# Kernel tuning notes

Measured on AMD Instinct MI355X. Metric: run time of the kernel, lower is better.

## Reference

```python
import jax, jax.numpy as jnp
import numpy as np

N_NODES = 200_000
N_EDGES = 6_400_000
N_GRAPHS = 512


def _sage_conv(x, edge_index, Wl, bl, Wr):
    """PyG SAGEConv (mean aggr): lin_l(mean_j x_j) + lin_r(x_i).
    lin_l has bias, lin_r does not. Messages flow src -> dst."""
    src, dst = edge_index[0], edge_index[1]
    n = x.shape[0]
    # gather neighbor features [E, F] and segment-mean into dst nodes
    msg_sum = jax.ops.segment_sum(x[src], dst, num_segments=n)
    deg = jax.ops.segment_sum(jnp.ones((src.shape[0],), x.dtype), dst, num_segments=n)
    mean = msg_sum / jnp.maximum(deg, 1.0)[:, None]  # zero in-degree -> 0
    return mean @ Wl.T + bl + x @ Wr.T


def setup_inputs() -> dict:
    key = jax.random.key(0)
    ks = jax.random.split(key, 9)
    x = jax.random.normal(ks[0], (N_NODES, 1), dtype=jnp.float32)
    edge_index = jax.random.randint(ks[1], (2, N_EDGES), 0, N_NODES, dtype=jnp.int64)
    batch = jnp.sort(jax.random.randint(ks[2], (N_NODES,), 0, N_GRAPHS, dtype=jnp.int64))
    W1l = jax.random.normal(ks[3], (16, 1), dtype=jnp.float32)
    b1 = jax.random.normal(ks[4], (16,), dtype=jnp.float32)
    W1r = jax.random.normal(ks[5], (16, 1), dtype=jnp.float32)
    W2l = jax.random.normal(ks[6], (1, 16), dtype=jnp.float32)
    b2 = jax.random.normal(ks[7], (1,), dtype=jnp.float32)
    W2r = jax.random.normal(ks[8], (1, 16), dtype=jnp.float32)
    return {"x": x, "edge_index": edge_index, "batch": batch, "batch_size": N_GRAPHS,
            "W1l": W1l, "b1": b1, "W1r": W1r, "W2l": W2l, "b2": b2, "W2r": W2r}


def reference(x, edge_index, batch, batch_size, W1l, b1, W1r, W2l, b2, W2r):
    h = _sage_conv(x, edge_index, W1l, b1, W1r)          # [N, 16]
    h = jax.nn.relu(h)
    h = _sage_conv(h, edge_index, W2l, b2, W2r)          # [N, 1]
    # global_add_pool: segment-sum node features by graph id
    out = jax.ops.segment_sum(h, batch, num_segments=batch_size)  # [B, 1]
    return out
```

## Files before the change

### kernel.cpp

```cpp
#include <hip/hip_runtime.h>


#define PARTS     512
#define BLK       1024
#define EPT       8
#define TILE      (BLK * EPT)
#define PGRID     512
#define BINSMAX   400
#define LDSHIFT   9
#define LDMASK    511u
#define CNT_ONE   (1u << 25)
#define FX_BIAS   131072
#define SCALE     4096.0f
#define INV_SCALE (1.0f / 4096.0f)

__global__ __launch_bounds__(BLK) void partition_kernel(
    const int* __restrict__ ei, unsigned* __restrict__ pairs,
    unsigned* __restrict__ tails, int E, int bins, unsigned Mdiv, int cap,
    int T) {
    __shared__ unsigned hist[PARTS], curs[PARTS], gbase[PARTS];
    const int tid = threadIdx.x;

    for (int t = blockIdx.x; t < T; t += PGRID) {
        for (int j = tid; j < PARTS; j += BLK) { hist[j] = 0; curs[j] = 0; }
        __syncthreads();

        int eb = t * TILE + tid * EPT;
        int nv = E - eb; nv = nv < 0 ? 0 : (nv > EPT ? EPT : nv);
        int srcv[EPT], dstv[EPT];
        if (nv == EPT && ((E & 3) == 0)) {
            const int4* s4 = (const int4*)(ei + eb);
            const int4* d4 = (const int4*)(ei + E + eb);
            int4 a = s4[0], b = s4[1];
            srcv[0] = a.x; srcv[1] = a.y; srcv[2] = a.z; srcv[3] = a.w;
            srcv[4] = b.x; srcv[5] = b.y; srcv[6] = b.z; srcv[7] = b.w;
            int4 c = d4[0], d = d4[1];
            dstv[0] = c.x; dstv[1] = c.y; dstv[2] = c.z; dstv[3] = c.w;
            dstv[4] = d.x; dstv[5] = d.y; dstv[6] = d.z; dstv[7] = d.w;
        } else {
            for (int k = 0; k < nv; ++k) {
                srcv[k] = ei[eb + k]; dstv[k] = ei[E + eb + k];
            }
        }

        unsigned w[EPT]; int pt[EPT];
#pragma unroll
        for (int k = 0; k < EPT; ++k) {
            if (k < nv) {
                unsigned dst = (unsigned)dstv[k];
                unsigned pp = (unsigned)(((unsigned long long)dst * Mdiv) >> 32);
                int ld = (int)dst - (int)pp * bins;
                while (ld >= bins) { ld -= bins; ++pp; }
                while (ld < 0)     { ld += bins; --pp; }
                pt[k] = (int)pp;
                w[k] = ((unsigned)srcv[k] << LDSHIFT) | (unsigned)ld;
                atomicAdd(&hist[pp], 1u);
            }
        }
        __syncthreads();

        if (tid < PARTS) {
            unsigned h = hist[tid];
            gbase[tid] = h ? atomicAdd(&tails[tid], h) : 0u;
        }
        __syncthreads();

#pragma unroll
        for (int k = 0; k < EPT; ++k) {
            if (k < nv) {
                unsigned slot = atomicAdd(&curs[pt[k]], 1u);
                unsigned idx = gbase[pt[k]] + slot;
                if (idx < (unsigned)cap)
                    pairs[(size_t)pt[k] * cap + idx] = w[k];
            }
        }
        __syncthreads();
    }
}

__global__ __launch_bounds__(BLK) void bin1_kernel(
    const unsigned* __restrict__ pairs, const unsigned* __restrict__ tails,
    const float* __restrict__ x,
    const float* __restrict__ W1l, const float* __restrict__ b1,
    const float* __restrict__ W1r, const float* __restrict__ W2l,
    const float* __restrict__ W2r,
    float* __restrict__ deg, float* __restrict__ pv, float* __restrict__ qv,
    int N, int bins, int cap) {
    __shared__ unsigned sb[BINSMAX];
    __shared__ float s_w1l[16], s_b1[16], s_w1r[16], s_w2l[16], s_w2r[16];
    const int tid = threadIdx.x;
    const int p = blockIdx.x;
    if (tid < 16) {
        s_w1l[tid] = W1l[tid]; s_b1[tid] = b1[tid]; s_w1r[tid] = W1r[tid];
        s_w2l[tid] = W2l[tid]; s_w2r[tid] = W2r[tid];
    }
    for (int j = tid; j < bins; j += BLK) sb[j] = 0;
    __syncthreads();

    int len = (int)tails[p]; if (len > cap) len = cap;
    const unsigned* bp = pairs + (size_t)p * cap;
    int n4 = len >> 2;
    const uint4* bp4 = (const uint4*)bp;
    for (int e = tid; e < n4; e += BLK) {
        uint4 wq = bp4[e];
        atomicAdd(&sb[wq.x & LDMASK],
                  CNT_ONE + (unsigned)((int)rintf(x[wq.x >> LDSHIFT] * SCALE) + FX_BIAS));
        atomicAdd(&sb[wq.y & LDMASK],
                  CNT_ONE + (unsigned)((int)rintf(x[wq.y >> LDSHIFT] * SCALE) + FX_BIAS));
        atomicAdd(&sb[wq.z & LDMASK],
                  CNT_ONE + (unsigned)((int)rintf(x[wq.z >> LDSHIFT] * SCALE) + FX_BIAS));
        atomicAdd(&sb[wq.w & LDMASK],
                  CNT_ONE + (unsigned)((int)rintf(x[wq.w >> LDSHIFT] * SCALE) + FX_BIAS));
    }
    for (int e = (n4 << 2) + tid; e < len; e += BLK) {
        unsigned wv = bp[e];
        atomicAdd(&sb[wv & LDMASK],
                  CNT_ONE + (unsigned)((int)rintf(x[wv >> LDSHIFT] * SCALE) + FX_BIAS));
    }
    __syncthreads();

    int lo = p * bins;
    int nb = N - lo; if (nb > bins) nb = bins;
    for (int j = tid; j < nb; j += BLK) {
        unsigned w = sb[j];
        unsigned c = w >> 25;
        float dg  = (float)c;
        float sum = (float)(int)((w & (CNT_ONE - 1)) - c * (unsigned)FX_BIAS) * INV_SCALE;
        float m   = sum / fmaxf(dg, 1.0f);
        float xv  = x[lo + j];
        float pa = 0.0f, qa = 0.0f;
#pragma unroll
        for (int f = 0; f < 16; ++f) {
            float h = fmaf(m, s_w1l[f], fmaf(xv, s_w1r[f], s_b1[f]));
            h = fmaxf(h, 0.0f);
            pa = fmaf(h, s_w2l[f], pa);
            qa = fmaf(h, s_w2r[f], qa);
        }
        deg[lo + j] = dg;
        pv[lo + j]  = pa;
        qv[lo + j]  = qa;
    }
}

__global__ __launch_bounds__(BLK) void bin2_kernel(
    const unsigned* __restrict__ pairs, const unsigned* __restrict__ tails,
    const float* __restrict__ pv, const float* __restrict__ deg,
    const float* __restrict__ qv, const float* __restrict__ b2,
    const int* __restrict__ batch, float* __restrict__ out,
    int N, int bins, int cap) {
    __shared__ int sbi[BINSMAX];
    const int tid = threadIdx.x;
    const int p = blockIdx.x;
    for (int j = tid; j < bins; j += BLK) sbi[j] = 0;
    __syncthreads();

    int len = (int)tails[p]; if (len > cap) len = cap;
    const unsigned* bp = pairs + (size_t)p * cap;
    int n4 = len >> 2;
    const uint4* bp4 = (const uint4*)bp;
    for (int e = tid; e < n4; e += BLK) {
        uint4 wq = bp4[e];
        atomicAdd(&sbi[wq.x & LDMASK], (int)rintf(pv[wq.x >> LDSHIFT] * SCALE));
        atomicAdd(&sbi[wq.y & LDMASK], (int)rintf(pv[wq.y >> LDSHIFT] * SCALE));
        atomicAdd(&sbi[wq.z & LDMASK], (int)rintf(pv[wq.z >> LDSHIFT] * SCALE));
        atomicAdd(&sbi[wq.w & LDMASK], (int)rintf(pv[wq.w >> LDSHIFT] * SCALE));
    }
    for (int e = (n4 << 2) + tid; e < len; e += BLK) {
        unsigned wv = bp[e];
        atomicAdd(&sbi[wv & LDMASK], (int)rintf(pv[wv >> LDSHIFT] * SCALE));
    }
    __syncthreads();

    int lo = p * bins;
    int nb = N - lo; if (nb > bins) nb = bins;
    float b2v = b2[0];
    float val = 0.0f;
    int g;
    if (tid < nb) {
        float s2 = (float)sbi[tid] * INV_SCALE;
        val = s2 / fmaxf(deg[lo + tid], 1.0f) + b2v + qv[lo + tid];
        g = batch[lo + tid];
    } else {
        g = batch[lo + nb - 1];
    }
    int g0 = __shfl(g, 0);
    unsigned long long same = __ballot(g == g0);
    if (same == ~0ULL) {
        for (int off = 32; off > 0; off >>= 1) val += __shfl_down(val, off);
        if ((tid & 63) == 0) atomicAdd(&out[g0], val);
    } else {
        atomicAdd(&out[g], val);
    }
}

extern "C" void kernel_launch(void* const* d_in, const int* in_sizes, int n_in,
                              void* d_out, int out_size, void* d_ws, size_t ws_size,
                              hipStream_t stream) {
    const float* x     = (const float*)d_in[0];
    const int*   ei    = (const int*)d_in[1];
    const int*   batch = (const int*)d_in[2];
    const float* W1l = (const float*)d_in[4];
    const float* b1  = (const float*)d_in[5];
    const float* W1r = (const float*)d_in[6];
    const float* W2l = (const float*)d_in[7];
    const float* b2  = (const float*)d_in[8];
    const float* W2r = (const float*)d_in[9];

    const int N = in_sizes[0];
    const int E = in_sizes[1] / 2;
    float* out = (float*)d_out;

    const int bins = (N + PARTS - 1) / PARTS;
    const unsigned Mdiv =
        (unsigned)(((1ULL << 32) + (unsigned)bins - 1) / (unsigned)bins);
    const int EperP = E / PARTS;
    int cap = ((EperP + EperP / 8 + 1024) + 1023) & ~1023;
    int T = (E + TILE - 1) / TILE;

    unsigned* pairs = (unsigned*)d_ws;
    float* deg = (float*)(pairs + (size_t)PARTS * cap);
    float* pv  = deg + N;
    float* qv  = pv + N;
    unsigned* tails = (unsigned*)(qv + N);

    hipMemsetAsync(d_out, 0, (size_t)out_size * sizeof(float), stream);
    hipMemsetAsync(tails, 0, PARTS * sizeof(unsigned), stream);

    partition_kernel<<<PGRID, BLK, 0, stream>>>(ei, pairs, tails,
                                                E, bins, Mdiv, cap, T);
    bin1_kernel<<<PARTS, BLK, 0, stream>>>(pairs, tails, x, W1l, b1, W1r,
                                           W2l, W2r, deg, pv, qv, N, bins, cap);
    bin2_kernel<<<PARTS, BLK, 0, stream>>>(pairs, tails, pv, deg, qv, b2,
                                           batch, out, N, bins, cap);
}
```

Measured before the change: 243.3 us.

## Embed quantized source features during partition and halve partition count

The partition pass now gathers x for each edge's source and stores a 16-bit biased fixed-point copy next to the packed edge word. Layer-1 binning then streams these values instead of doing random gathers into x. Partitions drop from 512 to 256, which doubles the bin width, and the remaining gather loops in both binning kernels are unrolled to 8 edges per thread. The per-partition capacity now comes from the workspace size, with a fallback to the old gather path; in exchange the partition pass does extra writes and x values are clamped to a 16-bit range.

```diff
diff --git a/kernel.cpp b/kernel.cpp
--- a/kernel.cpp
+++ b/kernel.cpp
@@ -1,21 +1,23 @@
 #include <hip/hip_runtime.h>
 
 
-#define PARTS     512
+#define PARTS     256
 #define BLK       1024
 #define EPT       8
 #define TILE      (BLK * EPT)
-#define PGRID     512
-#define BINSMAX   400
-#define LDSHIFT   9
-#define LDMASK    511u
+#define PGRID     256
+#define BINSMAX   800
+#define LDSHIFT   10
+#define LDMASK    1023u
 #define CNT_ONE   (1u << 25)
+#define XV_BIAS   32768
 #define FX_BIAS   131072
 #define SCALE     4096.0f
 #define INV_SCALE (1.0f / 4096.0f)
 
-__global__ __launch_bounds__(BLK) void partition_kernel(
-    const int* __restrict__ ei, unsigned* __restrict__ pairs,
+__global__ __launch_bounds__(BLK) void partition_embed_kernel(
+    const int* __restrict__ ei, const float* __restrict__ x,
+    unsigned* __restrict__ pairs, unsigned short* __restrict__ xvs,
     unsigned* __restrict__ tails, int E, int bins, unsigned Mdiv, int cap,
     int T) {
     __shared__ unsigned hist[PARTS], curs[PARTS], gbase[PARTS];
@@ -43,6 +45,10 @@
             }
         }
 
+        float xg[EPT];
+#pragma unroll
+        for (int k = 0; k < EPT; ++k) if (k < nv) xg[k] = x[srcv[k]];
+
         unsigned w[EPT]; int pt[EPT];
 #pragma unroll
         for (int k = 0; k < EPT; ++k) {
@@ -70,6 +76,70 @@
             if (k < nv) {
                 unsigned slot = atomicAdd(&curs[pt[k]], 1u);
                 unsigned idx = gbase[pt[k]] + slot;
+                if (idx < (unsigned)cap) {
+                    int xq = (int)rintf(xg[k] * SCALE) + XV_BIAS;
+                    xq = xq < 0 ? 0 : (xq > 65535 ? 65535 : xq);
+                    size_t o = (size_t)pt[k] * cap + idx;
+                    pairs[o] = w[k];
+                    xvs[o] = (unsigned short)xq;
+                }
+            }
+        }
+        __syncthreads();
+    }
+}
+
+__global__ __launch_bounds__(BLK) void partition_plain_kernel(
+    const int* __restrict__ ei, unsigned* __restrict__ pairs,
+    unsigned* __restrict__ tails, int E, int bins, unsigned Mdiv, int cap,
+    int T) {
+    __shared__ unsigned hist[PARTS], curs[PARTS], gbase[PARTS];
+    const int tid = threadIdx.x;
+    for (int t = blockIdx.x; t < T; t += PGRID) {
+        for (int j = tid; j < PARTS; j += BLK) { hist[j] = 0; curs[j] = 0; }
+        __syncthreads();
+        int eb = t * TILE + tid * EPT;
+        int nv = E - eb; nv = nv < 0 ? 0 : (nv > EPT ? EPT : nv);
+        int srcv[EPT], dstv[EPT];
+        if (nv == EPT && ((E & 3) == 0)) {
+            const int4* s4 = (const int4*)(ei + eb);
+            const int4* d4 = (const int4*)(ei + E + eb);
+            int4 a = s4[0], b = s4[1];
+            srcv[0] = a.x; srcv[1] = a.y; srcv[2] = a.z; srcv[3] = a.w;
+            srcv[4] = b.x; srcv[5] = b.y; srcv[6] = b.z; srcv[7] = b.w;
+            int4 c = d4[0], d = d4[1];
+            dstv[0] = c.x; dstv[1] = c.y; dstv[2] = c.z; dstv[3] = c.w;
+            dstv[4] = d.x; dstv[5] = d.y; dstv[6] = d.z; dstv[7] = d.w;
+        } else {
+            for (int k = 0; k < nv; ++k) {
+                srcv[k] = ei[eb + k]; dstv[k] = ei[E + eb + k];
+            }
+        }
+        unsigned w[EPT]; int pt[EPT];
+#pragma unroll
+        for (int k = 0; k < EPT; ++k) {
+            if (k < nv) {
+                unsigned dst = (unsigned)dstv[k];
+                unsigned pp = (unsigned)(((unsigned long long)dst * Mdiv) >> 32);
+                int ld = (int)dst - (int)pp * bins;
+                while (ld >= bins) { ld -= bins; ++pp; }
+                while (ld < 0)     { ld += bins; --pp; }
+                pt[k] = (int)pp;
+                w[k] = ((unsigned)srcv[k] << LDSHIFT) | (unsigned)ld;
+                atomicAdd(&hist[pp], 1u);
+            }
+        }
+        __syncthreads();
+        if (tid < PARTS) {
+            unsigned h = hist[tid];
+            gbase[tid] = h ? atomicAdd(&tails[tid], h) : 0u;
+        }
+        __syncthreads();
+#pragma unroll
+        for (int k = 0; k < EPT; ++k) {
+            if (k < nv) {
+                unsigned slot = atomicAdd(&curs[pt[k]], 1u);
+                unsigned idx = gbase[pt[k]] + slot;
                 if (idx < (unsigned)cap)
                     pairs[(size_t)pt[k] * cap + idx] = w[k];
             }
@@ -78,7 +148,78 @@
     }
 }
 
-__global__ __launch_bounds__(BLK) void bin1_kernel(
+__device__ __forceinline__ void node_phase1(
+    const unsigned* sb, const float* x,
+    const float* s_w1l, const float* s_b1, const float* s_w1r,
+    const float* s_w2l, const float* s_w2r,
+    float* deg, float* pv, float* qv, int lo, int nb, int bias) {
+    for (int j = threadIdx.x; j < nb; j += BLK) {
+        unsigned w = sb[j];
+        unsigned c = w >> 25;
+        float dg  = (float)c;
+        float sum = (float)((int)(w & (CNT_ONE - 1)) - (int)(c * (unsigned)bias))
+                    * INV_SCALE;
+        float m   = sum / fmaxf(dg, 1.0f);
+        float xv  = x[lo + j];
+        float pa = 0.0f, qa = 0.0f;
+#pragma unroll
+        for (int f = 0; f < 16; ++f) {
+            float h = fmaf(m, s_w1l[f], fmaf(xv, s_w1r[f], s_b1[f]));
+            h = fmaxf(h, 0.0f);
+            pa = fmaf(h, s_w2l[f], pa);
+            qa = fmaf(h, s_w2r[f], qa);
+        }
+        deg[lo + j] = dg;
+        pv[lo + j]  = pa;
+        qv[lo + j]  = qa;
+    }
+}
+
+__global__ __launch_bounds__(BLK) void bin1_stream_kernel(
+    const unsigned* __restrict__ pairs, const unsigned short* __restrict__ xvs,
+    const unsigned* __restrict__ tails, const float* __restrict__ x,
+    const float* __restrict__ W1l, const float* __restrict__ b1,
+    const float* __restrict__ W1r, const float* __restrict__ W2l,
+    const float* __restrict__ W2r,
+    float* __restrict__ deg, float* __restrict__ pv, float* __restrict__ qv,
+    int N, int bins, int cap) {
+    __shared__ unsigned sb[BINSMAX];
+    __shared__ float s_w1l[16], s_b1[16], s_w1r[16], s_w2l[16], s_w2r[16];
+    const int tid = threadIdx.x;
+    const int p = blockIdx.x;
+    if (tid < 16) {
+        s_w1l[tid] = W1l[tid]; s_b1[tid] = b1[tid]; s_w1r[tid] = W1r[tid];
+        s_w2l[tid] = W2l[tid]; s_w2r[tid] = W2r[tid];
+    }
+    for (int j = tid; j < bins; j += BLK) sb[j] = 0;
+    __syncthreads();
+
+    int len = (int)tails[p]; if (len > cap) len = cap;
+    const unsigned* bp = pairs + (size_t)p * cap;
+    const unsigned short* xp = xvs + (size_t)p * cap;
+    int n4 = len >> 2;
+    const uint4* bp4 = (const uint4*)bp;
+    const ushort4* xp4 = (const ushort4*)xp;
+    for (int e = tid; e < n4; e += BLK) {
+        uint4 wq = bp4[e];
+        ushort4 xw = xp4[e];
+        atomicAdd(&sb[wq.x & LDMASK], CNT_ONE + (unsigned)xw.x);
+        atomicAdd(&sb[wq.y & LDMASK], CNT_ONE + (unsigned)xw.y);
+        atomicAdd(&sb[wq.z & LDMASK], CNT_ONE + (unsigned)xw.z);
+        atomicAdd(&sb[wq.w & LDMASK], CNT_ONE + (unsigned)xw.w);
+    }
+    for (int e = (n4 << 2) + tid; e < len; e += BLK) {
+        atomicAdd(&sb[bp[e] & LDMASK], CNT_ONE + (unsigned)xp[e]);
+    }
+    __syncthreads();
+
+    int lo = p * bins;
+    int nb = N - lo; if (nb > bins) nb = bins;
+    node_phase1(sb, x, s_w1l, s_b1, s_w1r, s_w2l, s_w2r,
+                deg, pv, qv, lo, nb, XV_BIAS);
+}
+
+__global__ __launch_bounds__(BLK) void bin1_gather_kernel(
     const unsigned* __restrict__ pairs, const unsigned* __restrict__ tails,
     const float* __restrict__ x,
     const float* __restrict__ W1l, const float* __restrict__ b1,
@@ -99,20 +240,24 @@
 
     int len = (int)tails[p]; if (len > cap) len = cap;
     const unsigned* bp = pairs + (size_t)p * cap;
-    int n4 = len >> 2;
+    int n8 = len >> 3;
     const uint4* bp4 = (const uint4*)bp;
-    for (int e = tid; e < n4; e += BLK) {
-        uint4 wq = bp4[e];
-        atomicAdd(&sb[wq.x & LDMASK],
-                  CNT_ONE + (unsigned)((int)rintf(x[wq.x >> LDSHIFT] * SCALE) + FX_BIAS));
-        atomicAdd(&sb[wq.y & LDMASK],
-                  CNT_ONE + (unsigned)((int)rintf(x[wq.y >> LDSHIFT] * SCALE) + FX_BIAS));
-        atomicAdd(&sb[wq.z & LDMASK],
-                  CNT_ONE + (unsigned)((int)rintf(x[wq.z >> LDSHIFT] * SCALE) + FX_BIAS));
-        atomicAdd(&sb[wq.w & LDMASK],
-                  CNT_ONE + (unsigned)((int)rintf(x[wq.w >> LDSHIFT] * SCALE) + FX_BIAS));
-    }
-    for (int e = (n4 << 2) + tid; e < len; e += BLK) {
+    for (int i = tid; i < n8; i += BLK) {
+        uint4 a = bp4[2 * i], b = bp4[2 * i + 1];
+        float v0 = x[a.x >> LDSHIFT], v1 = x[a.y >> LDSHIFT];
+        float v2 = x[a.z >> LDSHIFT], v3 = x[a.w >> LDSHIFT];
+        float v4 = x[b.x >> LDSHIFT], v5 = x[b.y >> LDSHIFT];
+        float v6 = x[b.z >> LDSHIFT], v7 = x[b.w >> LDSHIFT];
+        atomicAdd(&sb[a.x & LDMASK], CNT_ONE + (unsigned)((int)rintf(v0 * SCALE) + FX_BIAS));
+        atomicAdd(&sb[a.y & LDMASK], CNT_ONE + (unsigned)((int)rintf(v1 * SCALE) + FX_BIAS));
+        atomicAdd(&sb[a.z & LDMASK], CNT_ONE + (unsigned)((int)rintf(v2 * SCALE) + FX_BIAS));
+        atomicAdd(&sb[a.w & LDMASK], CNT_ONE + (unsigned)((int)rintf(v3 * SCALE) + FX_BIAS));
+        atomicAdd(&sb[b.x & LDMASK], CNT_ONE + (unsigned)((int)rintf(v4 * SCALE) + FX_BIAS));
+        atomicAdd(&sb[b.y & LDMASK], CNT_ONE + (unsigned)((int)rintf(v5 * SCALE) + FX_BIAS));
+        atomicAdd(&sb[b.z & LDMASK], CNT_ONE + (unsigned)((int)rintf(v6 * SCALE) + FX_BIAS));
+        atomicAdd(&sb[b.w & LDMASK], CNT_ONE + (unsigned)((int)rintf(v7 * SCALE) + FX_BIAS));
+    }
+    for (int e = (n8 << 3) + tid; e < len; e += BLK) {
         unsigned wv = bp[e];
         atomicAdd(&sb[wv & LDMASK],
                   CNT_ONE + (unsigned)((int)rintf(x[wv >> LDSHIFT] * SCALE) + FX_BIAS));
@@ -121,25 +266,8 @@
 
     int lo = p * bins;
     int nb = N - lo; if (nb > bins) nb = bins;
-    for (int j = tid; j < nb; j += BLK) {
-        unsigned w = sb[j];
-        unsigned c = w >> 25;
-        float dg  = (float)c;
-        float sum = (float)(int)((w & (CNT_ONE - 1)) - c * (unsigned)FX_BIAS) * INV_SCALE;
-        float m   = sum / fmaxf(dg, 1.0f);
-        float xv  = x[lo + j];
-        float pa = 0.0f, qa = 0.0f;
-#pragma unroll
-        for (int f = 0; f < 16; ++f) {
-            float h = fmaf(m, s_w1l[f], fmaf(xv, s_w1r[f], s_b1[f]));
-            h = fmaxf(h, 0.0f);
-            pa = fmaf(h, s_w2l[f], pa);
-            qa = fmaf(h, s_w2r[f], qa);
-        }
-        deg[lo + j] = dg;
-        pv[lo + j]  = pa;
-        qv[lo + j]  = qa;
-    }
+    node_phase1(sb, x, s_w1l, s_b1, s_w1r, s_w2l, s_w2r,
+                deg, pv, qv, lo, nb, FX_BIAS);
 }
 
 __global__ __launch_bounds__(BLK) void bin2_kernel(
@@ -156,16 +284,24 @@
 
     int len = (int)tails[p]; if (len > cap) len = cap;
     const unsigned* bp = pairs + (size_t)p * cap;
-    int n4 = len >> 2;
+    int n8 = len >> 3;
     const uint4* bp4 = (const uint4*)bp;
-    for (int e = tid; e < n4; e += BLK) {
-        uint4 wq = bp4[e];
-        atomicAdd(&sbi[wq.x & LDMASK], (int)rintf(pv[wq.x >> LDSHIFT] * SCALE));
-        atomicAdd(&sbi[wq.y & LDMASK], (int)rintf(pv[wq.y >> LDSHIFT] * SCALE));
-        atomicAdd(&sbi[wq.z & LDMASK], (int)rintf(pv[wq.z >> LDSHIFT] * SCALE));
-        atomicAdd(&sbi[wq.w & LDMASK], (int)rintf(pv[wq.w >> LDSHIFT] * SCALE));
-    }
-    for (int e = (n4 << 2) + tid; e < len; e += BLK) {
+    for (int i = tid; i < n8; i += BLK) {
+        uint4 a = bp4[2 * i], b = bp4[2 * i + 1];
+        float v0 = pv[a.x >> LDSHIFT], v1 = pv[a.y >> LDSHIFT];
+        float v2 = pv[a.z >> LDSHIFT], v3 = pv[a.w >> LDSHIFT];
+        float v4 = pv[b.x >> LDSHIFT], v5 = pv[b.y >> LDSHIFT];
+        float v6 = pv[b.z >> LDSHIFT], v7 = pv[b.w >> LDSHIFT];
+        atomicAdd(&sbi[a.x & LDMASK], (int)rintf(v0 * SCALE));
+        atomicAdd(&sbi[a.y & LDMASK], (int)rintf(v1 * SCALE));
+        atomicAdd(&sbi[a.z & LDMASK], (int)rintf(v2 * SCALE));
+        atomicAdd(&sbi[a.w & LDMASK], (int)rintf(v3 * SCALE));
+        atomicAdd(&sbi[b.x & LDMASK], (int)rintf(v4 * SCALE));
+        atomicAdd(&sbi[b.y & LDMASK], (int)rintf(v5 * SCALE));
+        atomicAdd(&sbi[b.z & LDMASK], (int)rintf(v6 * SCALE));
+        atomicAdd(&sbi[b.w & LDMASK], (int)rintf(v7 * SCALE));
+    }
+    for (int e = (n8 << 3) + tid; e < len; e += BLK) {
         unsigned wv = bp[e];
         atomicAdd(&sbi[wv & LDMASK], (int)rintf(pv[wv >> LDSHIFT] * SCALE));
     }
@@ -213,12 +349,25 @@
     const int bins = (N + PARTS - 1) / PARTS;
     const unsigned Mdiv =
         (unsigned)(((1ULL << 32) + (unsigned)bins - 1) / (unsigned)bins);
-    const int EperP = E / PARTS;
-    int cap = ((EperP + EperP / 8 + 1024) + 1023) & ~1023;
     int T = (E + TILE - 1) / TILE;
 
+    long long wsWords = (long long)(ws_size / 4);
+    long long avail = wsWords - (3LL * N + 1024);
+    int capE = (int)((avail / 384) * 256) & ~1023;
+    capE = (int)((avail * 2 / 3) / PARTS) & ~1023;
+    bool embed = capE >= 26624;
+    int cap;
+    if (embed) {
+        cap = capE > 30720 ? 30720 : capE;
+    } else {
+        cap = (int)(avail / PARTS) & ~1023;
+        if (cap > 30720) cap = 30720;
+    }
+
     unsigned* pairs = (unsigned*)d_ws;
-    float* deg = (float*)(pairs + (size_t)PARTS * cap);
+    unsigned short* xvs = (unsigned short*)(pairs + (size_t)PARTS * cap);
+    float* deg = embed ? (float*)(xvs + (size_t)PARTS * cap)
+                       : (float*)(pairs + (size_t)PARTS * cap);
     float* pv  = deg + N;
     float* qv  = pv + N;
     unsigned* tails = (unsigned*)(qv + N);
@@ -226,10 +375,19 @@
     hipMemsetAsync(d_out, 0, (size_t)out_size * sizeof(float), stream);
     hipMemsetAsync(tails, 0, PARTS * sizeof(unsigned), stream);
 
-    partition_kernel<<<PGRID, BLK, 0, stream>>>(ei, pairs, tails,
-                                                E, bins, Mdiv, cap, T);
-    bin1_kernel<<<PARTS, BLK, 0, stream>>>(pairs, tails, x, W1l, b1, W1r,
-                                           W2l, W2r, deg, pv, qv, N, bins, cap);
+    if (embed) {
+        partition_embed_kernel<<<PGRID, BLK, 0, stream>>>(
+            ei, x, pairs, xvs, tails, E, bins, Mdiv, cap, T);
+        bin1_stream_kernel<<<PARTS, BLK, 0, stream>>>(
+            pairs, xvs, tails, x, W1l, b1, W1r, W2l, W2r,
+            deg, pv, qv, N, bins, cap);
+    } else {
+        partition_plain_kernel<<<PGRID, BLK, 0, stream>>>(
+            ei, pairs, tails, E, bins, Mdiv, cap, T);
+        bin1_gather_kernel<<<PARTS, BLK, 0, stream>>>(
+            pairs, tails, x, W1l, b1, W1r, W2l, W2r,
+            deg, pv, qv, N, bins, cap);
+    }
     bin2_kernel<<<PARTS, BLK, 0, stream>>>(pairs, tails, pv, deg, qv, b2,
                                            batch, out, N, bins, cap);
 }
```

Result: slower. 266.5 us (+9.5%).
